# Kernel tuning notes

Measured on AMD Instinct MI355X. Metric: run time of the kernel, lower is better.

Reference implementation:

```python
import jax, jax.numpy as jnp
import numpy as np

B, S_IMG, S_TXT, H, D = 1, 2048, 512, 24, 128
HID = H * D  # 3072
S_TOT = S_TXT + S_IMG
IP_SCALE = 1.0
EPS = 1e-5


def setup_inputs() -> dict:
    key = jax.random.key(0)
    ks = jax.random.split(key, 16)
    r = lambda k, s: jax.random.normal(k, s, dtype=jnp.float32)
    w = lambda k, s: r(k, s) * 0.02
    theta = r(ks[15], (S_TOT, D))  # rotary angles over joint sequence
    z = lambda: jnp.zeros((HID,), jnp.float32)
    return dict(
        hidden_states=r(ks[0], (B, S_IMG, HID)),
        encoder_hidden_states=r(ks[1], (B, S_TXT, HID)),
        image_emb=r(ks[2], (B, 4, HID)),
        rope_cos=jnp.cos(theta), rope_sin=jnp.sin(theta),
        Wq=w(ks[3], (HID, HID)), bq=z(),
        Wk=w(ks[4], (HID, HID)), bk=z(),
        Wv=w(ks[5], (HID, HID)), bv=z(),
        Waq=w(ks[6], (HID, HID)), baq=z(),
        Wak=w(ks[7], (HID, HID)), bak=z(),
        Wav=w(ks[8], (HID, HID)), bav=z(),
        Wk_ip=w(ks[9], (HID, HID)),
        Wv_ip=w(ks[10], (HID, HID)),
        Wo=w(ks[11], (HID, HID)), bo=z(),
        Wao=w(ks[12], (HID, HID)), bao=z(),
    )


def _heads(x):  # [B,S,HID] -> [B,H,S,D]
    return x.reshape(x.shape[0], x.shape[1], H, D).transpose(0, 2, 1, 3)


def _unheads(x):  # [B,H,S,D] -> [B,S,HID]
    return x.transpose(0, 2, 1, 3).reshape(x.shape[0], x.shape[2], HID)


def _rmsnorm(x):  # over last dim, no affine (RMSNorm(128, affine=False))
    return x * jax.lax.rsqrt(jnp.mean(x * x, axis=-1, keepdims=True) + EPS)


def _rope(x, cos, sin):  # diffusers apply_rotary_emb, use_real, interleaved pairs
    xp = x.reshape(*x.shape[:-1], D // 2, 2)
    rot = jnp.stack([-xp[..., 1], xp[..., 0]], axis=-1).reshape(x.shape)
    return x * cos + rot * sin  # cos/sin [S,D] broadcast over [B,H,S,D]


def _sdpa(q, k, v):
    s = jnp.einsum('bhqd,bhkd->bhqk', q, k) / jnp.sqrt(jnp.asarray(D, q.dtype))
    return jnp.einsum('bhqk,bhkd->bhqd', jax.nn.softmax(s, axis=-1), v)


def _forward(hidden_states, encoder_hidden_states, image_emb, rope_cos, rope_sin,
             Wq, bq, Wk, bk, Wv, bv, Waq, baq, Wak, bak, Wav, bav,
             Wk_ip, Wv_ip, Wo, bo, Wao, bao):
    # main QKV over image-latent tokens
    q = _rmsnorm(_heads(hidden_states @ Wq.T + bq))
    k = _rmsnorm(_heads(hidden_states @ Wk.T + bk))
    v = _heads(hidden_states @ Wv.T + bv)
    # IP-adapter cross attention (query = latent q, kv from image_emb)
    k_ip = _rmsnorm(_heads(image_emb @ Wk_ip.T))
    v_ip = _heads(image_emb @ Wv_ip.T)
    ip_out = _unheads(_sdpa(q, k_ip, v_ip))  # [B,S_IMG,HID]
    # encoder (text) QKV, concat text-first as in Flux
    eq = _rmsnorm(_heads(encoder_hidden_states @ Waq.T + baq))
    ek = _rmsnorm(_heads(encoder_hidden_states @ Wak.T + bak))
    ev = _heads(encoder_hidden_states @ Wav.T + bav)
    q = jnp.concatenate([eq, q], axis=2)
    k = jnp.concatenate([ek, k], axis=2)
    v = jnp.concatenate([ev, v], axis=2)
    q = _rope(q, rope_cos, rope_sin)
    k = _rope(k, rope_cos, rope_sin)
    out = _unheads(_sdpa(q, k, v))  # [B,S_TOT,HID]
    enc_out, hid_out = out[:, :S_TXT], out[:, S_TXT:]
    hid_out = hid_out + IP_SCALE * ip_out
    hid_out = hid_out @ Wo.T + bo   # to_out[0] (+ identity dropout)
    enc_out = enc_out @ Wao.T + bao  # to_add_out
    return hid_out, enc_out


def reference(hidden_states, encoder_hidden_states, image_emb, rope_cos, rope_sin,
              Wq, bq, Wk, bk, Wv, bv, Waq, baq, Wak, bak, Wav, bav,
              Wk_ip, Wv_ip, Wo, bo, Wao, bao):
    return _forward(hidden_states, encoder_hidden_states, image_emb, rope_cos, rope_sin,
                    Wq, bq, Wk, bk, Wv, bv, Waq, baq, Wak, bak, Wav, bav,
                    Wk_ip, Wv_ip, Wo, bo, Wao, bao)
```

## Files before the change

kernel.cpp:

```cpp
#include <hip/hip_runtime.h>

typedef __bf16 bf16;
typedef __bf16 bf16x2 __attribute__((ext_vector_type(2)));
typedef __bf16 bf16x4 __attribute__((ext_vector_type(4)));
typedef __bf16 bf16x8 __attribute__((ext_vector_type(8)));
typedef float  f32x4  __attribute__((ext_vector_type(4)));

#define H_    24
#define D_    128
#define HID_  3072
#define SIMG_ 2048
#define STXT_ 512
#define STOT_ 2560
#define EPS_  1e-5f
#define SCALE_ 0.08838834764831845f
#define HH_   ((size_t)HID_*HID_)

typedef __attribute__((address_space(3))) unsigned int lds_uint;
typedef const __attribute__((address_space(1))) unsigned int glb_uint;
__device__ __forceinline__ void gll16(const void* g, void* l){
  __builtin_amdgcn_global_load_lds((glb_uint*)g, (lds_uint*)l, 16, 0, 0);
}

__device__ inline bf16x8 frag8f(const float* __restrict__ p){
  const f32x4 a = *(const f32x4*)p;
  const f32x4 b = *(const f32x4*)(p + 4);
  bf16x8 r;
  r[0]=(bf16)a[0]; r[1]=(bf16)a[1]; r[2]=(bf16)a[2]; r[3]=(bf16)a[3];
  r[4]=(bf16)b[0]; r[5]=(bf16)b[1]; r[6]=(bf16)b[2]; r[7]=(bf16)b[3];
  return r;
}

__device__ __forceinline__ void cvt8(const float* __restrict__ s, bf16* __restrict__ d, int i){
  const f32x4 a = *(const f32x4*)(s + i);
  const f32x4 b = *(const f32x4*)(s + i + 4);
  bf16x8 o;
  o[0]=(bf16)a[0]; o[1]=(bf16)a[1]; o[2]=(bf16)a[2]; o[3]=(bf16)a[3];
  o[4]=(bf16)b[0]; o[5]=(bf16)b[1]; o[6]=(bf16)b[2]; o[7]=(bf16)b[3];
  *(bf16x8*)(d + i) = o;
}

__global__ __launch_bounds__(256) void k_prep(
    const float* __restrict__ HS, const float* __restrict__ ENC,
    const float* __restrict__ W0, const float* __restrict__ W1,
    const float* __restrict__ W2, const float* __restrict__ W3,
    const float* __restrict__ W4, const float* __restrict__ W5,
    const float* __restrict__ W6, const float* __restrict__ W7,
    const float* __restrict__ IMG,
    const float* __restrict__ Wkip, const float* __restrict__ Wvip,
    bf16* __restrict__ HSb, bf16* __restrict__ ENCb, bf16* __restrict__ Wb8,
    bf16* __restrict__ rawKip, bf16* __restrict__ rawVip)
{
  const int bx = (int)blockIdx.x;
  if (bx < 3072){
    cvt8(HS, HSb, (bx*256 + (int)threadIdx.x)*8);
  } else if (bx < 3840){
    cvt8(ENC, ENCb, ((bx - 3072)*256 + (int)threadIdx.x)*8);
  } else if (bx < 40704){
    const int idx = bx - 3840;
    const int wi = idx / 4608;
    const float* s = (wi==0)?W0:(wi==1)?W1:(wi==2)?W2:(wi==3)?W3:(wi==4)?W4:(wi==5)?W5:(wi==6)?W6:W7;
    cvt8(s, Wb8 + (size_t)wi*HH_, ((idx % 4608)*256 + (int)threadIdx.x)*8);
  } else {
    const int bi = bx - 40704;
    const float* Wm = (bi >= 48) ? Wvip : Wkip;
    bf16* C = (bi >= 48) ? rawVip : rawKip;
    const int w = (int)(threadIdx.x >> 6), l = (int)(threadIdx.x & 63u);
    const int lr = l & 15, lg = l >> 4;
    const int nbw = (bi % 48)*64 + w*16;
    f32x4 acc = {};
    const float* arow = IMG + (size_t)((lr < 4) ? lr : 0)*HID_;
    const float* wrow = Wm + (size_t)(nbw + lr)*HID_;
    for (int k0 = 0; k0 < HID_; k0 += 32){
      const bf16x8 af  = frag8f(arow + k0 + lg*8);
      const bf16x8 bfr = frag8f(wrow + k0 + lg*8);
      acc = __builtin_amdgcn_mfma_f32_16x16x32_bf16(af, bfr, acc, 0, 0, 0);
    }
    if (lg == 0){
      #pragma unroll
      for (int r = 0; r < 4; r++)
        C[(size_t)r*HID_ + nbw + lr] = (bf16)acc[r];
    }
  }
}

#define MFMA_ __builtin_amdgcn_mfma_f32_16x16x32_bf16
#define MM(bfr, n) \
    acc[0][n]=MFMA_(af0,bfr,acc[0][n],0,0,0); acc[1][n]=MFMA_(af1,bfr,acc[1][n],0,0,0); \
    acc[2][n]=MFMA_(af2,bfr,acc[2][n],0,0,0); acc[3][n]=MFMA_(af3,bfr,acc[3][n],0,0,0);
#define WAIT6  asm volatile("s_waitcnt vmcnt(6)" ::: "memory")
#define WAIT0  asm volatile("s_waitcnt vmcnt(0)" ::: "memory")
#define NOWAIT (void)0

__device__ __forceinline__ void gemm8_core(
    const bf16* __restrict__ A, const bf16* __restrict__ W,
    int mb, int nb,
    f32x4 (&acc)[4][4],
    bf16 (&Al)[3][128][64],
    bf16 (&Bl)[3][256][64])
{
  const int t = (int)threadIdx.x;
  const int w = t >> 6, l = t & 63;
  const int lr = l & 15, lg = l >> 4;
  const int wr = w >> 2, wc = w & 3;
  const int srow = t >> 3;
  const int soff = ((t & 7) ^ (srow & 7)) * 8;

  const bf16* Abase = A + (size_t)(mb + srow)*HID_ + soff;
  const bf16* Wbase = W + (size_t)(nb + srow)*HID_ + soff;

#define SA(buf, tt, i) gll16(Abase + (size_t)(i)*64*HID_ + (tt)*64, &Al[buf][0][0] + (i)*4096 + t*8)
#define SB(buf, tt, i) gll16(Wbase + (size_t)(i)*64*HID_ + (tt)*64, &Bl[buf][0][0] + (i)*4096 + t*8)

  const int arow_ = wr*64 + lr;
  const int brow_ = wc*64 + lr;
  const int sx = lr & 7;

  SA(0,0,0); SA(0,0,1); SB(0,0,0); SB(0,0,1); SB(0,0,2); SB(0,0,3);
  SA(1,1,0); SA(1,1,1); SB(1,1,0); SB(1,1,1); SB(1,1,2); SB(1,1,3);
  WAIT6;
  __builtin_amdgcn_s_barrier();

#define TILE(C, NXT, TT, PRE, TW)                                            \
  {                                                                          \
    const int s0_ = (lg^sx)*8, s1_ = ((4+lg)^sx)*8;                          \
    bf16x8 af0,af1,af2,af3,b0,b1;                                            \
    af0=*(const bf16x8*)&Al[C][arow_   ][s0_];                               \
    af1=*(const bf16x8*)&Al[C][arow_+16][s0_];                               \
    af2=*(const bf16x8*)&Al[C][arow_+32][s0_];                               \
    af3=*(const bf16x8*)&Al[C][arow_+48][s0_];                               \
    b0 =*(const bf16x8*)&Bl[C][brow_   ][s0_];                               \
    b1 =*(const bf16x8*)&Bl[C][brow_+16][s0_];                               \
    if (PRE){ SA(NXT,(TT)+2,0); SA(NXT,(TT)+2,1); }                          \
    __builtin_amdgcn_s_setprio(1); MM(b0,0) MM(b1,1)                         \
    __builtin_amdgcn_s_setprio(0);                                           \
    b0 =*(const bf16x8*)&Bl[C][brow_+32][s0_];                               \
    b1 =*(const bf16x8*)&Bl[C][brow_+48][s0_];                               \
    if (PRE){ SB(NXT,(TT)+2,0); SB(NXT,(TT)+2,1); }                          \
    __builtin_amdgcn_s_setprio(1); MM(b0,2) MM(b1,3)                         \
    __builtin_amdgcn_s_setprio(0);                                           \
    af0=*(const bf16x8*)&Al[C][arow_   ][s1_];                               \
    af1=*(const bf16x8*)&Al[C][arow_+16][s1_];                               \
    af2=*(const bf16x8*)&Al[C][arow_+32][s1_];                               \
    af3=*(const bf16x8*)&Al[C][arow_+48][s1_];                               \
    b0 =*(const bf16x8*)&Bl[C][brow_   ][s1_];                               \
    b1 =*(const bf16x8*)&Bl[C][brow_+16][s1_];                               \
    if (PRE){ SB(NXT,(TT)+2,2); SB(NXT,(TT)+2,3); }                          \
    __builtin_amdgcn_s_setprio(1); MM(b0,0) MM(b1,1)                         \
    __builtin_amdgcn_s_setprio(0);                                           \
    b0 =*(const bf16x8*)&Bl[C][brow_+32][s1_];                               \
    b1 =*(const bf16x8*)&Bl[C][brow_+48][s1_];                               \
    __builtin_amdgcn_s_setprio(1); MM(b0,2) MM(b1,3)                         \
    __builtin_amdgcn_s_setprio(0);                                           \
    TW;                                                                      \
    __builtin_amdgcn_s_barrier();                                            \
  }

  for (int base = 0; base < 45; base += 3){
    TILE(0, 2, base,   true, WAIT6);
    TILE(1, 0, base+1, true, WAIT6);
    TILE(2, 1, base+2, true, WAIT6);
  }
  TILE(0, 2, 45, true,  WAIT6);
  TILE(1, 0, 46, false, WAIT0);
  TILE(2, 1, 47, false, NOWAIT);
#undef TILE
#undef SA
#undef SB
}

__global__ __launch_bounds__(512, 1) void k_gemm8_qkv(
    const bf16* __restrict__ Ahid, const bf16* __restrict__ Aenc,
    const bf16* __restrict__ Wb,
    const float* bq, const float* bk, const float* bv,
    const float* baq, const float* bak, const float* bav,
    bf16* Cq, bf16* Ck, bf16* Cv, bf16* Ceq, bf16* Cek, bf16* Cev)
{
  __shared__ __align__(16) bf16 Al[3][128][64];
  __shared__ __align__(16) bf16 Bl[3][256][64];
  const int lin = (int)blockIdx.x;
  const int work = (lin & 7)*90 + (lin >> 3);
  const int mt = work / 36;
  const int ct = work % 36;
  const int which = ct % 3;
  const int nb = (ct/3)*256;
  const int enc = (mt >= 16) ? 1 : 0;
  const int mb = (enc ? (mt - 16) : mt)*128;
  const bf16* A = enc ? Aenc : Ahid;
  const int widx = which + enc*3;
  const bf16* W = Wb + (size_t)widx*HH_;
  const float* bias = (which==0) ? (enc?baq:bq) : (which==1) ? (enc?bak:bk) : (enc?bav:bv);
  bf16* Cm = (which==0) ? (enc?Ceq:Cq) : (which==1) ? (enc?Cek:Ck) : (enc?Cev:Cv);

  f32x4 acc[4][4] = {};
  gemm8_core(A, W, mb, nb, acc, Al, Bl);

  const int w = (int)(threadIdx.x >> 6), l = (int)(threadIdx.x & 63u);
  const int lr = l & 15, lg = l >> 4;
  const int wr = w >> 2, wc = w & 3;
  #pragma unroll
  for (int nf = 0; nf < 4; nf++){
    const int col = nb + wc*64 + nf*16 + lr;
    const float bvl = bias[col];
    #pragma unroll
    for (int m = 0; m < 4; m++){
      #pragma unroll
      for (int r = 0; r < 4; r++){
        const int row = mb + wr*64 + m*16 + lg*4 + r;
        Cm[(size_t)row*HID_ + col] = (bf16)(acc[m][nf][r] + bvl);
      }
    }
  }
}

__global__ __launch_bounds__(512, 1) void k_gemm8_out(
    const bf16* __restrict__ Ahid, const bf16* __restrict__ Aenc,
    const bf16* __restrict__ Wb,
    const float* bo, const float* bao, float* __restrict__ outp)
{
  __shared__ __align__(16) bf16 Al[3][128][64];
  __shared__ __align__(16) bf16 Bl[3][256][64];
  const int lin = (int)blockIdx.x;
  const int work = (lin & 7)*30 + (lin >> 3);
  const int mt = work / 12;
  const int nb = (work % 12)*256;
  const int enc = (mt >= 16) ? 1 : 0;
  const int mb = (enc ? (mt - 16) : mt)*128;
  const bf16* A = enc ? Aenc : Ahid;
  const bf16* W = Wb + (size_t)(enc ? 7 : 6)*HH_;
  const float* bias = enc ? bao : bo;
  float* C = outp + (enc ? (size_t)SIMG_*HID_ : 0);

  f32x4 acc[4][4] = {};
  gemm8_core(A, W, mb, nb, acc, Al, Bl);

  const int w = (int)(threadIdx.x >> 6), l = (int)(threadIdx.x & 63u);
  const int lr = l & 15, lg = l >> 4;
  const int wr = w >> 2, wc = w & 3;
  #pragma unroll
  for (int nf = 0; nf < 4; nf++){
    const int col = nb + wc*64 + nf*16 + lr;
    const float bvl = bias[col];
    #pragma unroll
    for (int m = 0; m < 4; m++){
      #pragma unroll
      for (int r = 0; r < 4; r++){
        const int row = mb + wr*64 + m*16 + lg*4 + r;
        C[(size_t)row*HID_ + col] = acc[m][nf][r] + bvl;
      }
    }
  }
}

__global__ __launch_bounds__(256) void k_finish_all(
    const bf16* __restrict__ rawQ, const bf16* __restrict__ rawK, const bf16* __restrict__ rawV,
    const bf16* __restrict__ rawEQ, const bf16* __restrict__ rawEK, const bf16* __restrict__ rawEV,
    const float* __restrict__ cosT, const float* __restrict__ sinT,
    const bf16* __restrict__ rawKip, const bf16* __restrict__ rawVip,
    bf16* __restrict__ Qh, bf16* __restrict__ Kh, bf16* __restrict__ Vt,
    float* __restrict__ Kip, float* __restrict__ Vip)
{
  __shared__ bf16 lt[128*130];
  const int bx = (int)blockIdx.x;
  const int t = (int)threadIdx.x;
  if (bx < 15360){
    const int wid = bx*4 + (t >> 6);
    const int l = t & 63;
    const int s = wid / H_;
    const int h = wid % H_;
    const bf16 *sq_, *sk_;
    if (s < STXT_){
      const size_t off = (size_t)s*HID_ + h*D_;
      sq_ = rawEQ + off; sk_ = rawEK + off;
    } else {
      const size_t off = (size_t)(s - STXT_)*HID_ + h*D_;
      sq_ = rawQ + off; sk_ = rawK + off;
    }
    const int d0 = 2*l, d1 = 2*l + 1;
    float q0 = sq_[d0], q1 = sq_[d1];
    float k0 = sk_[d0], k1 = sk_[d1];
    float ssq = q0*q0 + q1*q1;
    float ssk = k0*k0 + k1*k1;
    #pragma unroll
    for (int m = 1; m < 64; m <<= 1){ ssq += __shfl_xor(ssq, m); ssk += __shfl_xor(ssk, m); }
    const float rq = rsqrtf(ssq*(1.0f/128.0f) + EPS_);
    const float rk = rsqrtf(ssk*(1.0f/128.0f) + EPS_);
    q0 *= rq; q1 *= rq; k0 *= rk; k1 *= rk;
    const float c0 = cosT[(size_t)s*D_ + d0], c1 = cosT[(size_t)s*D_ + d1];
    const float s0 = sinT[(size_t)s*D_ + d0], s1 = sinT[(size_t)s*D_ + d1];
    const float qo0 = q0*c0 - q1*s0, qo1 = q1*c1 + q0*s1;
    const float ko0 = k0*c0 - k1*s0, ko1 = k1*c1 + k0*s1;
    const size_t qoff = ((size_t)h*STOT_ + s)*D_ + d0;
    Qh[qoff] = (bf16)qo0; Qh[qoff + 1] = (bf16)qo1;
    Kh[qoff] = (bf16)ko0; Kh[qoff + 1] = (bf16)ko1;
  } else if (bx < 15840){
    const int v = bx - 15360;
    const int stile = (v % 20)*128;
    const int h = v / 20;
    #pragma unroll
    for (int i = 0; i < 8; i++){
      const int sl = i*16 + (t >> 4);
      const int s = stile + sl;
      const bf16* src = (s < STXT_) ? (rawEV + (size_t)s*HID_) : (rawV + (size_t)(s - STXT_)*HID_);
      const bf16x8 vv = *(const bf16x8*)(src + h*D_ + (t & 15)*8);
      #pragma unroll
      for (int j = 0; j < 8; j++) lt[((t & 15)*8 + j)*130 + sl] = vv[j];
    }
    __syncthreads();
    #pragma unroll
    for (int j = 0; j < 4; j++){
      const int d = j*32 + (t >> 3);
      const int s0 = (t & 7)*16;
      bf16x8 a, b;
      #pragma unroll
      for (int k = 0; k < 4; k++){
        const bf16x2 p = *(const bf16x2*)(lt + d*130 + s0 + 2*k);
        a[2*k] = p[0]; a[2*k+1] = p[1];
      }
      #pragma unroll
      for (int k = 0; k < 4; k++){
        const bf16x2 p = *(const bf16x2*)(lt + d*130 + s0 + 8 + 2*k);
        b[2*k] = p[0]; b[2*k+1] = p[1];
      }
      bf16* dst = Vt + ((size_t)h*D_ + d)*STOT_ + stile + s0;
      *(bf16x8*)dst = a;
      *(bf16x8*)(dst + 8) = b;
    }
  } else {
    const int wid = (bx - 15840)*4 + (t >> 6);
    const int l = t & 63;
    const int h = wid / 4, j = wid % 4;
    const int d0 = 2*l, d1 = 2*l + 1;
    const size_t src = (size_t)j*HID_ + h*D_;
    float k0 = rawKip[src + d0], k1 = rawKip[src + d1];
    float v0 = rawVip[src + d0], v1 = rawVip[src + d1];
    float ss = k0*k0 + k1*k1;
    #pragma unroll
    for (int m = 1; m < 64; m <<= 1) ss += __shfl_xor(ss, m);
    const float rk = rsqrtf(ss*(1.0f/128.0f) + EPS_);
    const size_t dst = ((size_t)h*4 + j)*D_;
    Kip[dst + d0] = k0*rk; Kip[dst + d1] = k1*rk;
    Vip[dst + d0] = v0;    Vip[dst + d1] = v1;
  }
}

__global__ __launch_bounds__(256) void k_ip_attn(
    const bf16* __restrict__ rawQ, const float* __restrict__ Kip,
    const float* __restrict__ Vip, bf16* __restrict__ ipOut)
{
  const int wid = (int)blockIdx.x*4 + (int)(threadIdx.x >> 6);
  const int l = (int)(threadIdx.x & 63u);
  const int s = wid / H_, h = wid % H_;
  const int d0 = 2*l, d1 = 2*l + 1;
  const bf16* src = rawQ + (size_t)s*HID_ + h*D_;
  float q0 = src[d0], q1 = src[d1];
  float ss = q0*q0 + q1*q1;
  #pragma unroll
  for (int m = 1; m < 64; m <<= 1) ss += __shfl_xor(ss, m);
  const float r = rsqrtf(ss*(1.0f/128.0f) + EPS_);
  q0 *= r; q1 *= r;
  const float* kb = Kip + (size_t)h*4*D_;
  const float* vb = Vip + (size_t)h*4*D_;
  float sc[4];
  #pragma unroll
  for (int j = 0; j < 4; j++) sc[j] = q0*kb[j*D_ + d0] + q1*kb[j*D_ + d1];
  #pragma unroll
  for (int m = 1; m < 64; m <<= 1){
    #pragma unroll
    for (int j = 0; j < 4; j++) sc[j] += __shfl_xor(sc[j], m);
  }
  const float mx = fmaxf(fmaxf(sc[0], sc[1]), fmaxf(sc[2], sc[3]));
  float p[4], ps = 0.f;
  #pragma unroll
  for (int j = 0; j < 4; j++){ p[j] = __expf((sc[j] - mx)*SCALE_); ps += p[j]; }
  const float inv = 1.0f/ps;
  float o0 = 0.f, o1 = 0.f;
  #pragma unroll
  for (int j = 0; j < 4; j++){ o0 += p[j]*vb[j*D_ + d0]; o1 += p[j]*vb[j*D_ + d1]; }
  const size_t dst = (size_t)s*HID_ + h*D_;
  ipOut[dst + d0] = (bf16)(o0*inv);
  ipOut[dst + d1] = (bf16)(o1*inv);
}

__global__ __launch_bounds__(256, 2) void k_flash3(
    const bf16* __restrict__ Q, const bf16* __restrict__ K,
    const bf16* __restrict__ Vt, const bf16* __restrict__ ipOut,
    bf16* __restrict__ attnOut)
{
  __shared__ __align__(16) bf16 Ks[2][64*128];
  __shared__ __align__(16) bf16 Vs[2][128*64];
  __shared__ __align__(16) bf16 plds[4][32*64];
  const int t = (int)threadIdx.x;
  const int w = t >> 6, l = t & 63;
  const int lr = l & 15, lg = l >> 4;
  const int lin = (int)blockIdx.x;
  const int work = (lin & 7)*60 + (lin >> 3);
  const int h = work / 20;
  const int qbase = (work % 20)*128 + w*32;
  const bf16* Qh = Q  + (size_t)h*STOT_*D_;
  const bf16* Kh = K  + (size_t)h*STOT_*D_;
  const bf16* Vh = Vt + (size_t)h*D_*STOT_;

  bf16x8 qf[2][4];
  #pragma unroll
  for (int qt = 0; qt < 2; qt++)
    #pragma unroll
    for (int kk = 0; kk < 4; kk++)
      qf[qt][kk] = *(const bf16x8*)(Qh + (size_t)(qbase + qt*16 + lr)*D_ + kk*32 + lg*8);

  f32x4 acc[2][8] = {};
  float mrun[2] = {-3.0e38f, -3.0e38f}, lrun[2] = {0.f, 0.f};

  const int krow = t >> 4, kslot = t & 15;
  const int vrow = t >> 3, vslot = t & 7;

  auto STAGE = [&](int buf, int kv){
    #pragma unroll
    for (int i = 0; i < 4; i++){
      const int r = i*16 + krow;
      gll16(Kh + (size_t)(kv + r)*D_ + ((kslot ^ (r & 7))*8),
            (void*)(&Ks[buf][0] + (size_t)t*8 + i*2048));
    }
    #pragma unroll
    for (int i = 0; i < 4; i++){
      const int r = i*32 + vrow;
      gll16(Vh + (size_t)r*STOT_ + kv + ((vslot ^ (r & 7))*8),
            (void*)(&Vs[buf][0] + (size_t)t*8 + i*2048));
    }
  };

  STAGE(0, 0);
  __syncthreads();
  int cur = 0;
  for (int kv = 0; kv < STOT_; kv += 64){
    if (kv + 64 < STOT_) STAGE(cur ^ 1, kv + 64);

    f32x4 st[2][4] = {};
    #pragma unroll
    for (int tt = 0; tt < 4; tt++){
      const int kr = tt*16 + lr;
      #pragma unroll
      for (int kk = 0; kk < 4; kk++){
        const bf16x8 kf = *(const bf16x8*)(&Ks[cur][0] + kr*128 + (((kk*4 + lg) ^ (kr & 7))*8));
        st[0][tt] = __builtin_amdgcn_mfma_f32_16x16x32_bf16(kf, qf[0][kk], st[0][tt], 0, 0, 0);
        st[1][tt] = __builtin_amdgcn_mfma_f32_16x16x32_bf16(kf, qf[1][kk], st[1][tt], 0, 0, 0);
      }
    }
    #pragma unroll
    for (int qt = 0; qt < 2; qt++){
      const int q = qt*16 + lr;
      float sv[4][4];
      float vmax = -3.0e38f;
      #pragma unroll
      for (int tt = 0; tt < 4; tt++)
        #pragma unroll
        for (int r = 0; r < 4; r++){ const float x = st[qt][tt][r]*SCALE_; sv[tt][r] = x; vmax = fmaxf(vmax, x); }
      vmax = fmaxf(vmax, __shfl_xor(vmax, 16));
      vmax = fmaxf(vmax, __shfl_xor(vmax, 32));
      const float mnew  = fmaxf(mrun[qt], vmax);
      const float alpha = __expf(mrun[qt] - mnew);
      float rs = 0.f;
      #pragma unroll
      for (int tt = 0; tt < 4; tt++){
        bf16x4 pq;
        #pragma unroll
        for (int r = 0; r < 4; r++){
          const float p = __expf(sv[tt][r] - mnew);
          rs += p;
          pq[r] = (bf16)p;
        }
        *(bf16x4*)(&plds[w][q*64 + (((tt*2 + (lg >> 1)) ^ (q & 7))*8) + (lg & 1)*4]) = pq;
      }
      rs += __shfl_xor(rs, 16);
      rs += __shfl_xor(rs, 32);
      lrun[qt] = lrun[qt]*alpha + rs;
      mrun[qt] = mnew;
      #pragma unroll
      for (int n = 0; n < 8; n++)
        #pragma unroll
        for (int r = 0; r < 4; r++) acc[qt][n][r] *= alpha;
    }
    #pragma unroll
    for (int ks = 0; ks < 2; ks++){
      const bf16x8 pb0 = *(const bf16x8*)(&plds[w][(lr)*64      + (((ks*4 + lg) ^ (lr & 7))*8)]);
      const bf16x8 pb1 = *(const bf16x8*)(&plds[w][(16 + lr)*64 + (((ks*4 + lg) ^ (lr & 7))*8)]);
      #pragma unroll
      for (int n = 0; n < 8; n++){
        const int vr = n*16 + lr;
        const bf16x8 vf = *(const bf16x8*)(&Vs[cur][0] + vr*64 + (((ks*4 + lg) ^ (vr & 7))*8));
        acc[0][n] = __builtin_amdgcn_mfma_f32_16x16x32_bf16(vf, pb0, acc[0][n], 0, 0, 0);
        acc[1][n] = __builtin_amdgcn_mfma_f32_16x16x32_bf16(vf, pb1, acc[1][n], 0, 0, 0);
      }
    }
    __syncthreads();
    cur ^= 1;
  }
  const bool hid = (qbase >= STXT_);
  #pragma unroll
  for (int qt = 0; qt < 2; qt++){
    const float inv = 1.0f/lrun[qt];
    const int row = qbase + qt*16 + lr;
    #pragma unroll
    for (int n = 0; n < 8; n++){
      const size_t cbase = (size_t)row*HID_ + h*D_ + n*16 + lg*4;
      if (hid){
        const bf16x4 ip = *(const bf16x4*)(ipOut + (size_t)(row - STXT_)*HID_ + h*D_ + n*16 + lg*4);
        bf16x4 o;
        #pragma unroll
        for (int r = 0; r < 4; r++) o[r] = (bf16)(acc[qt][n][r]*inv + (float)ip[r]);
        *(bf16x4*)(attnOut + cbase) = o;
      } else {
        bf16x4 o;
        #pragma unroll
        for (int r = 0; r < 4; r++) o[r] = (bf16)(acc[qt][n][r]*inv);
        *(bf16x4*)(attnOut + cbase) = o;
      }
    }
  }
}

extern "C" void kernel_launch(void* const* d_in, const int* in_sizes, int n_in,
                              void* d_out, int out_size, void* d_ws, size_t ws_size,
                              hipStream_t stream)
{
  const float* HS   = (const float*)d_in[0];
  const float* ENC  = (const float*)d_in[1];
  const float* IMG  = (const float*)d_in[2];
  const float* COS  = (const float*)d_in[3];
  const float* SIN  = (const float*)d_in[4];
  const float* Wq   = (const float*)d_in[5];  const float* bq  = (const float*)d_in[6];
  const float* Wk   = (const float*)d_in[7];  const float* bk  = (const float*)d_in[8];
  const float* Wv   = (const float*)d_in[9];  const float* bv  = (const float*)d_in[10];
  const float* Waq  = (const float*)d_in[11]; const float* baq = (const float*)d_in[12];
  const float* Wak  = (const float*)d_in[13]; const float* bak = (const float*)d_in[14];
  const float* Wav  = (const float*)d_in[15]; const float* bav = (const float*)d_in[16];
  const float* Wkip = (const float*)d_in[17]; const float* Wvip= (const float*)d_in[18];
  const float* Wo   = (const float*)d_in[19]; const float* bo  = (const float*)d_in[20];
  const float* Wao  = (const float*)d_in[21]; const float* bao = (const float*)d_in[22];

  char* wsb = (char*)d_ws;
  size_t off = 0;
  auto alloc = [&](size_t bytes) -> char* {
    char* p = wsb + off; off += (bytes + 255) & ~((size_t)255); return p;
  };
  bf16* rawQ   = (bf16*)alloc((size_t)SIMG_*HID_*2);
  bf16* rawK   = (bf16*)alloc((size_t)SIMG_*HID_*2);
  bf16* rawV   = (bf16*)alloc((size_t)SIMG_*HID_*2);
  bf16* rawEQ  = (bf16*)alloc((size_t)STXT_*HID_*2);
  bf16* rawEK  = (bf16*)alloc((size_t)STXT_*HID_*2);
  bf16* rawEV  = (bf16*)alloc((size_t)STXT_*HID_*2);
  bf16* rawKip = (bf16*)alloc((size_t)4*HID_*2);
  bf16* rawVip = (bf16*)alloc((size_t)4*HID_*2);
  bf16* Qb     = (bf16*)alloc((size_t)H_*STOT_*D_*2);
  bf16* Kb     = (bf16*)alloc((size_t)H_*STOT_*D_*2);
  bf16* Vtb    = (bf16*)alloc((size_t)H_*STOT_*D_*2);
  bf16* AOUT   = (bf16*)alloc((size_t)STOT_*HID_*2);
  bf16* IPOUT  = (bf16*)alloc((size_t)SIMG_*HID_*2);
  float* KIPF  = (float*)alloc((size_t)H_*4*D_*4);
  float* VIPF  = (float*)alloc((size_t)H_*4*D_*4);
  bf16* HSb    = (bf16*)alloc((size_t)SIMG_*HID_*2);
  bf16* ENCb   = (bf16*)alloc((size_t)STXT_*HID_*2);
  bf16* Wb8    = (bf16*)alloc((size_t)8*HH_*2);

  dim3 blk(256);
  dim3 blk512(512);
  k_prep<<<dim3(40800), blk, 0, stream>>>(HS, ENC, Wq, Wk, Wv, Waq, Wak, Wav, Wo, Wao,
                                          IMG, Wkip, Wvip, HSb, ENCb, Wb8, rawKip, rawVip);
  k_gemm8_qkv<<<dim3(720), blk512, 0, stream>>>(HSb, ENCb, Wb8,
                                                bq, bk, bv, baq, bak, bav,
                                                rawQ, rawK, rawV, rawEQ, rawEK, rawEV);
  k_finish_all<<<dim3(15864), blk, 0, stream>>>(rawQ, rawK, rawV, rawEQ, rawEK, rawEV,
                                                COS, SIN, rawKip, rawVip,
                                                Qb, Kb, Vtb, KIPF, VIPF);
  k_ip_attn<<<dim3(12288), blk, 0, stream>>>(rawQ, KIPF, VIPF, IPOUT);
  k_flash3<<<dim3(480), blk, 0, stream>>>(Qb, Kb, Vtb, IPOUT, AOUT);
  float* outp = (float*)d_out;
  k_gemm8_out<<<dim3(240), blk512, 0, stream>>>(AOUT + (size_t)STXT_*HID_, AOUT, Wb8, bo, bao, outp);
}
```

Before: 612.0 us.

## Fuse IP-adapter attention into QK finish kernel and finalize Kip/Vip in prep

The IP-adapter K/V projection in the prep kernel now computes a full head per block and writes the RMS-normalized Kip and Vip in fp32 directly, so no separate finish pass is needed. The per-token IP attention is merged into the Q/K norm+rope kernel, which reuses the already-normalized q values instead of rereading rawQ and re-normalizing. The V transpose moves to its own small kernel. This saves one global read of rawQ and removes a launch, at the cost of extra registers and work in the fused kernel and one more launch for the transpose.

```diff
diff --git a/kernel.cpp b/kernel.cpp
--- a/kernel.cpp
+++ b/kernel.cpp
@@ -49,37 +49,58 @@
     const float* __restrict__ IMG,
     const float* __restrict__ Wkip, const float* __restrict__ Wvip,
     bf16* __restrict__ HSb, bf16* __restrict__ ENCb, bf16* __restrict__ Wb8,
-    bf16* __restrict__ rawKip, bf16* __restrict__ rawVip)
-{
+    float* __restrict__ Kip, float* __restrict__ Vip)
+{
+  __shared__ float tile[4][128];
   const int bx = (int)blockIdx.x;
+  const int t = (int)threadIdx.x;
   if (bx < 3072){
-    cvt8(HS, HSb, (bx*256 + (int)threadIdx.x)*8);
+    cvt8(HS, HSb, (bx*256 + t)*8);
   } else if (bx < 3840){
-    cvt8(ENC, ENCb, ((bx - 3072)*256 + (int)threadIdx.x)*8);
+    cvt8(ENC, ENCb, ((bx - 3072)*256 + t)*8);
   } else if (bx < 40704){
     const int idx = bx - 3840;
     const int wi = idx / 4608;
     const float* s = (wi==0)?W0:(wi==1)?W1:(wi==2)?W2:(wi==3)?W3:(wi==4)?W4:(wi==5)?W5:(wi==6)?W6:W7;
-    cvt8(s, Wb8 + (size_t)wi*HH_, ((idx % 4608)*256 + (int)threadIdx.x)*8);
+    cvt8(s, Wb8 + (size_t)wi*HH_, ((idx % 4608)*256 + t)*8);
   } else {
     const int bi = bx - 40704;
-    const float* Wm = (bi >= 48) ? Wvip : Wkip;
-    bf16* C = (bi >= 48) ? rawVip : rawKip;
-    const int w = (int)(threadIdx.x >> 6), l = (int)(threadIdx.x & 63u);
+    const bool isV = (bi >= 24);
+    const int h = bi % 24;
+    const float* Wm = isV ? Wvip : Wkip;
+    const int w = t >> 6, l = t & 63;
     const int lr = l & 15, lg = l >> 4;
-    const int nbw = (bi % 48)*64 + w*16;
-    f32x4 acc = {};
+    const int col0 = h*128 + w*32;
+    f32x4 acc0 = {}, acc1 = {};
     const float* arow = IMG + (size_t)((lr < 4) ? lr : 0)*HID_;
-    const float* wrow = Wm + (size_t)(nbw + lr)*HID_;
+    const float* wr0 = Wm + (size_t)(col0 + lr)*HID_;
+    const float* wr1 = Wm + (size_t)(col0 + 16 + lr)*HID_;
     for (int k0 = 0; k0 < HID_; k0 += 32){
-      const bf16x8 af  = frag8f(arow + k0 + lg*8);
-      const bf16x8 bfr = frag8f(wrow + k0 + lg*8);
-      acc = __builtin_amdgcn_mfma_f32_16x16x32_bf16(af, bfr, acc, 0, 0, 0);
+      const bf16x8 af = frag8f(arow + k0 + lg*8);
+      acc0 = __builtin_amdgcn_mfma_f32_16x16x32_bf16(af, frag8f(wr0 + k0 + lg*8), acc0, 0, 0, 0);
+      acc1 = __builtin_amdgcn_mfma_f32_16x16x32_bf16(af, frag8f(wr1 + k0 + lg*8), acc1, 0, 0, 0);
     }
     if (lg == 0){
       #pragma unroll
-      for (int r = 0; r < 4; r++)
-        C[(size_t)r*HID_ + nbw + lr] = (bf16)acc[r];
+      for (int r = 0; r < 4; r++){
+        tile[r][w*32 + lr]      = acc0[r];
+        tile[r][w*32 + 16 + lr] = acc1[r];
+      }
+    }
+    __syncthreads();
+    if (isV){
+      const int e = t*2;
+      const int j = e >> 7, d = e & 127;
+      Vip[(size_t)(h*4 + j)*D_ + d]     = tile[j][d];
+      Vip[(size_t)(h*4 + j)*D_ + d + 1] = tile[j][d + 1];
+    } else {
+      const float v0 = tile[w][2*l], v1 = tile[w][2*l + 1];
+      float ss = v0*v0 + v1*v1;
+      #pragma unroll
+      for (int m = 1; m < 64; m <<= 1) ss += __shfl_xor(ss, m);
+      const float rk = rsqrtf(ss*(1.0f/128.0f) + EPS_);
+      Kip[(size_t)(h*4 + w)*D_ + 2*l]     = v0*rk;
+      Kip[(size_t)(h*4 + w)*D_ + 2*l + 1] = v1*rk;
     }
   }
 }
@@ -252,134 +273,105 @@
   }
 }
 
-__global__ __launch_bounds__(256) void k_finish_all(
-    const bf16* __restrict__ rawQ, const bf16* __restrict__ rawK, const bf16* __restrict__ rawV,
-    const bf16* __restrict__ rawEQ, const bf16* __restrict__ rawEK, const bf16* __restrict__ rawEV,
+__global__ __launch_bounds__(256) void k_finish_qk2(
+    const bf16* __restrict__ rawQ, const bf16* __restrict__ rawK,
+    const bf16* __restrict__ rawEQ, const bf16* __restrict__ rawEK,
     const float* __restrict__ cosT, const float* __restrict__ sinT,
-    const bf16* __restrict__ rawKip, const bf16* __restrict__ rawVip,
-    bf16* __restrict__ Qh, bf16* __restrict__ Kh, bf16* __restrict__ Vt,
-    float* __restrict__ Kip, float* __restrict__ Vip)
-{
-  __shared__ bf16 lt[128*130];
-  const int bx = (int)blockIdx.x;
-  const int t = (int)threadIdx.x;
-  if (bx < 15360){
-    const int wid = bx*4 + (t >> 6);
-    const int l = t & 63;
-    const int s = wid / H_;
-    const int h = wid % H_;
-    const bf16 *sq_, *sk_;
-    if (s < STXT_){
-      const size_t off = (size_t)s*HID_ + h*D_;
-      sq_ = rawEQ + off; sk_ = rawEK + off;
-    } else {
-      const size_t off = (size_t)(s - STXT_)*HID_ + h*D_;
-      sq_ = rawQ + off; sk_ = rawK + off;
-    }
-    const int d0 = 2*l, d1 = 2*l + 1;
-    float q0 = sq_[d0], q1 = sq_[d1];
-    float k0 = sk_[d0], k1 = sk_[d1];
-    float ssq = q0*q0 + q1*q1;
-    float ssk = k0*k0 + k1*k1;
-    #pragma unroll
-    for (int m = 1; m < 64; m <<= 1){ ssq += __shfl_xor(ssq, m); ssk += __shfl_xor(ssk, m); }
-    const float rq = rsqrtf(ssq*(1.0f/128.0f) + EPS_);
-    const float rk = rsqrtf(ssk*(1.0f/128.0f) + EPS_);
-    q0 *= rq; q1 *= rq; k0 *= rk; k1 *= rk;
-    const float c0 = cosT[(size_t)s*D_ + d0], c1 = cosT[(size_t)s*D_ + d1];
-    const float s0 = sinT[(size_t)s*D_ + d0], s1 = sinT[(size_t)s*D_ + d1];
-    const float qo0 = q0*c0 - q1*s0, qo1 = q1*c1 + q0*s1;
-    const float ko0 = k0*c0 - k1*s0, ko1 = k1*c1 + k0*s1;
-    const size_t qoff = ((size_t)h*STOT_ + s)*D_ + d0;
-    Qh[qoff] = (bf16)qo0; Qh[qoff + 1] = (bf16)qo1;
-    Kh[qoff] = (bf16)ko0; Kh[qoff + 1] = (bf16)ko1;
-  } else if (bx < 15840){
-    const int v = bx - 15360;
-    const int stile = (v % 20)*128;
-    const int h = v / 20;
-    #pragma unroll
-    for (int i = 0; i < 8; i++){
-      const int sl = i*16 + (t >> 4);
-      const int s = stile + sl;
-      const bf16* src = (s < STXT_) ? (rawEV + (size_t)s*HID_) : (rawV + (size_t)(s - STXT_)*HID_);
-      const bf16x8 vv = *(const bf16x8*)(src + h*D_ + (t & 15)*8);
-      #pragma unroll
-      for (int j = 0; j < 8; j++) lt[((t & 15)*8 + j)*130 + sl] = vv[j];
-    }
-    __syncthreads();
-    #pragma unroll
-    for (int j = 0; j < 4; j++){
-      const int d = j*32 + (t >> 3);
-      const int s0 = (t & 7)*16;
-      bf16x8 a, b;
-      #pragma unroll
-      for (int k = 0; k < 4; k++){
-        const bf16x2 p = *(const bf16x2*)(lt + d*130 + s0 + 2*k);
-        a[2*k] = p[0]; a[2*k+1] = p[1];
-      }
-      #pragma unroll
-      for (int k = 0; k < 4; k++){
-        const bf16x2 p = *(const bf16x2*)(lt + d*130 + s0 + 8 + 2*k);
-        b[2*k] = p[0]; b[2*k+1] = p[1];
-      }
-      bf16* dst = Vt + ((size_t)h*D_ + d)*STOT_ + stile + s0;
-      *(bf16x8*)dst = a;
-      *(bf16x8*)(dst + 8) = b;
-    }
-  } else {
-    const int wid = (bx - 15840)*4 + (t >> 6);
-    const int l = t & 63;
-    const int h = wid / 4, j = wid % 4;
-    const int d0 = 2*l, d1 = 2*l + 1;
-    const size_t src = (size_t)j*HID_ + h*D_;
-    float k0 = rawKip[src + d0], k1 = rawKip[src + d1];
-    float v0 = rawVip[src + d0], v1 = rawVip[src + d1];
-    float ss = k0*k0 + k1*k1;
-    #pragma unroll
-    for (int m = 1; m < 64; m <<= 1) ss += __shfl_xor(ss, m);
-    const float rk = rsqrtf(ss*(1.0f/128.0f) + EPS_);
-    const size_t dst = ((size_t)h*4 + j)*D_;
-    Kip[dst + d0] = k0*rk; Kip[dst + d1] = k1*rk;
-    Vip[dst + d0] = v0;    Vip[dst + d1] = v1;
-  }
-}
-
-__global__ __launch_bounds__(256) void k_ip_attn(
-    const bf16* __restrict__ rawQ, const float* __restrict__ Kip,
-    const float* __restrict__ Vip, bf16* __restrict__ ipOut)
+    const float* __restrict__ Kip, const float* __restrict__ Vip,
+    bf16* __restrict__ Qh, bf16* __restrict__ Kh, bf16* __restrict__ ipOut)
 {
   const int wid = (int)blockIdx.x*4 + (int)(threadIdx.x >> 6);
   const int l = (int)(threadIdx.x & 63u);
-  const int s = wid / H_, h = wid % H_;
+  const int s = wid / H_;
+  const int h = wid % H_;
+  const bf16 *sq_, *sk_;
+  if (s < STXT_){
+    const size_t off = (size_t)s*HID_ + h*D_;
+    sq_ = rawEQ + off; sk_ = rawEK + off;
+  } else {
+    const size_t off = (size_t)(s - STXT_)*HID_ + h*D_;
+    sq_ = rawQ + off; sk_ = rawK + off;
+  }
   const int d0 = 2*l, d1 = 2*l + 1;
-  const bf16* src = rawQ + (size_t)s*HID_ + h*D_;
-  float q0 = src[d0], q1 = src[d1];
-  float ss = q0*q0 + q1*q1;
-  #pragma unroll
-  for (int m = 1; m < 64; m <<= 1) ss += __shfl_xor(ss, m);
-  const float r = rsqrtf(ss*(1.0f/128.0f) + EPS_);
-  q0 *= r; q1 *= r;
-  const float* kb = Kip + (size_t)h*4*D_;
-  const float* vb = Vip + (size_t)h*4*D_;
-  float sc[4];
-  #pragma unroll
-  for (int j = 0; j < 4; j++) sc[j] = q0*kb[j*D_ + d0] + q1*kb[j*D_ + d1];
-  #pragma unroll
-  for (int m = 1; m < 64; m <<= 1){
-    #pragma unroll
-    for (int j = 0; j < 4; j++) sc[j] += __shfl_xor(sc[j], m);
-  }
-  const float mx = fmaxf(fmaxf(sc[0], sc[1]), fmaxf(sc[2], sc[3]));
-  float p[4], ps = 0.f;
-  #pragma unroll
-  for (int j = 0; j < 4; j++){ p[j] = __expf((sc[j] - mx)*SCALE_); ps += p[j]; }
-  const float inv = 1.0f/ps;
-  float o0 = 0.f, o1 = 0.f;
-  #pragma unroll
-  for (int j = 0; j < 4; j++){ o0 += p[j]*vb[j*D_ + d0]; o1 += p[j]*vb[j*D_ + d1]; }
-  const size_t dst = (size_t)s*HID_ + h*D_;
-  ipOut[dst + d0] = (bf16)(o0*inv);
-  ipOut[dst + d1] = (bf16)(o1*inv);
+  float q0 = sq_[d0], q1 = sq_[d1];
+  float k0 = sk_[d0], k1 = sk_[d1];
+  float ssq = q0*q0 + q1*q1;
+  float ssk = k0*k0 + k1*k1;
+  #pragma unroll
+  for (int m = 1; m < 64; m <<= 1){ ssq += __shfl_xor(ssq, m); ssk += __shfl_xor(ssk, m); }
+  const float rq = rsqrtf(ssq*(1.0f/128.0f) + EPS_);
+  const float rk = rsqrtf(ssk*(1.0f/128.0f) + EPS_);
+  q0 *= rq; q1 *= rq; k0 *= rk; k1 *= rk;
+  const float c0 = cosT[(size_t)s*D_ + d0], c1 = cosT[(size_t)s*D_ + d1];
+  const float s0 = sinT[(size_t)s*D_ + d0], s1 = sinT[(size_t)s*D_ + d1];
+  const float qo0 = q0*c0 - q1*s0, qo1 = q1*c1 + q0*s1;
+  const float ko0 = k0*c0 - k1*s0, ko1 = k1*c1 + k0*s1;
+  const size_t qoff = ((size_t)h*STOT_ + s)*D_ + d0;
+  Qh[qoff] = (bf16)qo0; Qh[qoff + 1] = (bf16)qo1;
+  Kh[qoff] = (bf16)ko0; Kh[qoff + 1] = (bf16)ko1;
+
+  if (s >= STXT_){
+    const float* kb = Kip + (size_t)h*4*D_;
+    const float* vb = Vip + (size_t)h*4*D_;
+    float sc[4];
+    #pragma unroll
+    for (int j = 0; j < 4; j++) sc[j] = q0*kb[j*D_ + d0] + q1*kb[j*D_ + d1];
+    #pragma unroll
+    for (int m = 1; m < 64; m <<= 1){
+      #pragma unroll
+      for (int j = 0; j < 4; j++) sc[j] += __shfl_xor(sc[j], m);
+    }
+    const float mx = fmaxf(fmaxf(sc[0], sc[1]), fmaxf(sc[2], sc[3]));
+    float p[4], ps = 0.f;
+    #pragma unroll
+    for (int j = 0; j < 4; j++){ p[j] = __expf((sc[j] - mx)*SCALE_); ps += p[j]; }
+    const float inv = 1.0f/ps;
+    float o0 = 0.f, o1 = 0.f;
+    #pragma unroll
+    for (int j = 0; j < 4; j++){ o0 += p[j]*vb[j*D_ + d0]; o1 += p[j]*vb[j*D_ + d1]; }
+    const size_t dst = (size_t)(s - STXT_)*HID_ + h*D_;
+    ipOut[dst + d0] = (bf16)(o0*inv);
+    ipOut[dst + d1] = (bf16)(o1*inv);
+  }
+}
+
+__global__ __launch_bounds__(256) void k_vtrans(
+    const bf16* __restrict__ rawV, const bf16* __restrict__ rawEV,
+    bf16* __restrict__ Vt)
+{
+  __shared__ bf16 lt[128*130];
+  const int t = (int)threadIdx.x;
+  const int stile = (int)blockIdx.x*128;
+  const int h = (int)blockIdx.y;
+  #pragma unroll
+  for (int i = 0; i < 8; i++){
+    const int sl = i*16 + (t >> 4);
+    const int s = stile + sl;
+    const bf16* src = (s < STXT_) ? (rawEV + (size_t)s*HID_) : (rawV + (size_t)(s - STXT_)*HID_);
+    const bf16x8 v = *(const bf16x8*)(src + h*D_ + (t & 15)*8);
+    #pragma unroll
+    for (int j = 0; j < 8; j++) lt[((t & 15)*8 + j)*130 + sl] = v[j];
+  }
+  __syncthreads();
+  #pragma unroll
+  for (int j = 0; j < 4; j++){
+    const int d = j*32 + (t >> 3);
+    const int s0 = (t & 7)*16;
+    bf16x8 a, b;
+    #pragma unroll
+    for (int k = 0; k < 4; k++){
+      const bf16x2 p = *(const bf16x2*)(lt + d*130 + s0 + 2*k);
+      a[2*k] = p[0]; a[2*k+1] = p[1];
+    }
+    #pragma unroll
+    for (int k = 0; k < 4; k++){
+      const bf16x2 p = *(const bf16x2*)(lt + d*130 + s0 + 8 + 2*k);
+      b[2*k] = p[0]; b[2*k+1] = p[1];
+    }
+    bf16* dst = Vt + ((size_t)h*D_ + d)*STOT_ + stile + s0;
+    *(bf16x8*)dst = a;
+    *(bf16x8*)(dst + 8) = b;
+  }
 }
 
 __global__ __launch_bounds__(256, 2) void k_flash3(
@@ -549,8 +541,6 @@
   bf16* rawEQ  = (bf16*)alloc((size_t)STXT_*HID_*2);
   bf16* rawEK  = (bf16*)alloc((size_t)STXT_*HID_*2);
   bf16* rawEV  = (bf16*)alloc((size_t)STXT_*HID_*2);
-  bf16* rawKip = (bf16*)alloc((size_t)4*HID_*2);
-  bf16* rawVip = (bf16*)alloc((size_t)4*HID_*2);
   bf16* Qb     = (bf16*)alloc((size_t)H_*STOT_*D_*2);
   bf16* Kb     = (bf16*)alloc((size_t)H_*STOT_*D_*2);
   bf16* Vtb    = (bf16*)alloc((size_t)H_*STOT_*D_*2);
@@ -564,15 +554,14 @@
 
   dim3 blk(256);
   dim3 blk512(512);
-  k_prep<<<dim3(40800), blk, 0, stream>>>(HS, ENC, Wq, Wk, Wv, Waq, Wak, Wav, Wo, Wao,
-                                          IMG, Wkip, Wvip, HSb, ENCb, Wb8, rawKip, rawVip);
+  k_prep<<<dim3(40752), blk, 0, stream>>>(HS, ENC, Wq, Wk, Wv, Waq, Wak, Wav, Wo, Wao,
+                                          IMG, Wkip, Wvip, HSb, ENCb, Wb8, KIPF, VIPF);
   k_gemm8_qkv<<<dim3(720), blk512, 0, stream>>>(HSb, ENCb, Wb8,
                                                 bq, bk, bv, baq, bak, bav,
                                                 rawQ, rawK, rawV, rawEQ, rawEK, rawEV);
-  k_finish_all<<<dim3(15864), blk, 0, stream>>>(rawQ, rawK, rawV, rawEQ, rawEK, rawEV,
-                                                COS, SIN, rawKip, rawVip,
-                                                Qb, Kb, Vtb, KIPF, VIPF);
-  k_ip_attn<<<dim3(12288), blk, 0, stream>>>(rawQ, KIPF, VIPF, IPOUT);
+  k_finish_qk2<<<dim3(15360), blk, 0, stream>>>(rawQ, rawK, rawEQ, rawEK, COS, SIN,
+                                                KIPF, VIPF, Qb, Kb, IPOUT);
+  k_vtrans<<<dim3(20,24), blk, 0, stream>>>(rawV, rawEV, Vtb);
   k_flash3<<<dim3(480), blk, 0, stream>>>(Qb, Kb, Vtb, IPOUT, AOUT);
   float* outp = (float*)d_out;
   k_gemm8_out<<<dim3(240), blk512, 0, stream>>>(AOUT + (size_t)STXT_*HID_, AOUT, Wb8, bo, bao, outp);
```

Result: no change. 612.8 us (+0.1%).
